# Kernel optimization log

Measured on AMD Instinct MI355X. Metric: run time of the kernel, lower is better.

Reference implementation:

```python
import jax, jax.numpy as jnp
import numpy as np
import math

D = 64  # attention_head_size (hidden_size=64, num_heads=1)
B, N, M = 4, 256, 256
LN_EPS = 1e-5


def setup_inputs() -> dict:
    key = jax.random.key(0)
    ks = jax.random.split(key, 12)
    s = 1.0 / math.sqrt(D)
    return {
        "hidden_states": jax.random.normal(ks[0], (B, N, D), jnp.float32),
        "structure_matrix": jax.random.normal(ks[1], (B, N, M, D), jnp.float32),
        "Wq": jax.random.normal(ks[2], (D, D), jnp.float32) * s,
        "bq": jnp.zeros((D,), jnp.float32),
        "Wk": jax.random.normal(ks[3], (D, D), jnp.float32) * s,
        "bk": jnp.zeros((D,), jnp.float32),
        "Wv": jax.random.normal(ks[4], (D, D), jnp.float32) * s,
        "bv": jnp.zeros((D,), jnp.float32),
        "Wo": jax.random.normal(ks[5], (D, D), jnp.float32) * s,
        "bo": jnp.zeros((D,), jnp.float32),
        "ln_g": jnp.ones((D,), jnp.float32),
        "ln_b": jnp.zeros((D,), jnp.float32),
    }


def reference(hidden_states, structure_matrix, Wq, bq, Wk, bk, Wv, bv, Wo, bo, ln_g, ln_b):
    # hidden_states is unused by the original forward.
    x = structure_matrix  # [B, N, M, D]
    q = x @ Wq.T + bq
    k = x @ Wk.T + bk
    v = x @ Wv.T + bv
    # scores[b,i,a,c] = sum_d k[b,i,a,d] * q[b,i,c,d]  (query broadcast on axis 2)
    scores = jnp.einsum('biad,bicd->biac', k, q) / math.sqrt(D)
    probs = jax.nn.relu(scores)
    # NOTE: original sums (probs + 1e-12) so denom = sum(probs) + M*1e-12
    probs = probs / jnp.sum(probs + 1e-12, axis=-1, keepdims=True)
    # ctx[b,i,a,d] = sum_c probs[b,i,a,c] * v[b,i,c,d]
    ctx = jnp.einsum('biac,bicd->biad', probs, v)
    out = ctx @ Wo.T + bo
    y = out + x
    mu = jnp.mean(y, axis=-1, keepdims=True)
    var = jnp.mean(jnp.square(y - mu), axis=-1, keepdims=True)
    return (y - mu) / jnp.sqrt(var + LN_EPS) * ln_g + ln_b
```

## Files before the change

### kernel.cpp

```cpp
#include <hip/hip_runtime.h>


using bh8   = __attribute__((ext_vector_type(8))) short;
using f32x4 = __attribute__((ext_vector_type(4))) float;

#define MFMA(a, b, c) __builtin_amdgcn_mfma_f32_16x16x32_bf16((a), (b), (c), 0, 0, 0)

#define SQ_STRIDE  72
#define SVT_STRIDE 264
#define SY_STRIDE  72
#define STG_ELTS   (16 * 72)
#define LDS_BYTES  ((256 * SQ_STRIDE * 2 + 64 * SVT_STRIDE + 4 * STG_ELTS) * 2)

__device__ __forceinline__ float bf2f(unsigned short u) {
  union { unsigned int i; float f; } x;
  x.i = ((unsigned int)u) << 16;
  return x.f;
}
__device__ __forceinline__ unsigned short f2bf(float f) {
  union { float f; unsigned int i; } x;
  x.f = f;
  unsigned int u = x.i + 0x7FFFu + ((x.i >> 16) & 1u);
  return (unsigned short)(u >> 16);
}
__device__ __forceinline__ int pkbf(float lo, float hi) {
  return (int)(((unsigned int)f2bf(hi) << 16) | (unsigned int)f2bf(lo));
}

template <int FP32>
__device__ __forceinline__ bh8 g_load8(const void* base, size_t idx) {
  if constexpr (FP32) {
    const float* p = (const float*)base + idx;
    float4 a = *(const float4*)p;
    float4 b = *(const float4*)(p + 4);
    bh8 r;
    r[0] = (short)f2bf(a.x); r[1] = (short)f2bf(a.y);
    r[2] = (short)f2bf(a.z); r[3] = (short)f2bf(a.w);
    r[4] = (short)f2bf(b.x); r[5] = (short)f2bf(b.y);
    r[6] = (short)f2bf(b.z); r[7] = (short)f2bf(b.w);
    return r;
  } else {
    return *(const bh8*)((const unsigned short*)base + idx);
  }
}
template <int FP32>
__device__ __forceinline__ float g_loadf(const void* base, size_t idx) {
  if constexpr (FP32) return ((const float*)base)[idx];
  else return bf2f(((const unsigned short*)base)[idx]);
}

template <int FP32>
__global__ __launch_bounds__(256, 1) void pairattn(
    const void* __restrict__ Xv,
    const void* __restrict__ Wqv, const void* __restrict__ bqv,
    const void* __restrict__ Wkv, const void* __restrict__ bkv,
    const void* __restrict__ Wvv, const void* __restrict__ bvv,
    const void* __restrict__ Wov, const void* __restrict__ bov,
    const void* __restrict__ lngv, const void* __restrict__ lnbv,
    void* __restrict__ Outv) {
  const int tid  = threadIdx.x;
  const int lane = tid & 63;

  {
    const unsigned short* xu = (const unsigned short*)Xv + (lane << 4);
    int huge = 0;
#pragma unroll
    for (int j = 0; j < 16; ++j) {
      unsigned e = ((unsigned)xu[j] >> 7) & 0xFFu;
      huge |= (e >= 0x90u) ? 1 : 0;
    }
    const bool isf32 = (__ballot(huge) != 0ULL);
    if (isf32 != (FP32 != 0)) return;
  }

  extern __shared__ unsigned short sm[];
  unsigned short* sQ  = sm;
  unsigned short* sK  = sQ + 256 * SQ_STRIDE;
  unsigned short* sVt = sK + 256 * SQ_STRIDE;
  unsigned short* sSt = sVt + 64 * SVT_STRIDE;

  const int wv  = tid >> 6;
  const int q4  = lane >> 4;
  const int l16 = lane & 15;
  const int m0w = wv << 6;
  unsigned short* stg = sSt + wv * STG_ELTS;

  bh8 wq[4][2], wk[4][2], wvv[4][2], wo[4][2];
  float bqf[4], bkf[4], bvf[4][4], bof[4], gf[4], lbf[4];
#pragma unroll
  for (int nt = 0; nt < 4; ++nt) {
    const int wrow = (16 * nt + l16) * 64 + 8 * q4;
    wq[nt][0]  = g_load8<FP32>(Wqv, wrow);
    wq[nt][1]  = g_load8<FP32>(Wqv, wrow + 32);
    wk[nt][0]  = g_load8<FP32>(Wkv, wrow);
    wk[nt][1]  = g_load8<FP32>(Wkv, wrow + 32);
    wvv[nt][0] = g_load8<FP32>(Wvv, wrow);
    wvv[nt][1] = g_load8<FP32>(Wvv, wrow + 32);
    wo[nt][0]  = g_load8<FP32>(Wov, wrow);
    wo[nt][1]  = g_load8<FP32>(Wov, wrow + 32);
    const int col = 16 * nt + l16;
    bqf[nt] = g_loadf<FP32>(bqv, col);
    bkf[nt] = g_loadf<FP32>(bkv, col);
    bof[nt] = g_loadf<FP32>(bov, col);
    gf[nt]  = g_loadf<FP32>(lngv, col);
    lbf[nt] = g_loadf<FP32>(lnbv, col);
#pragma unroll
    for (int r = 0; r < 4; ++r)
      bvf[nt][r] = g_loadf<FP32>(bvv, 16 * nt + 4 * q4 + r);
  }

  const int srcA = ((lane & 16) << 1) | l16;
  const int srcB = srcA + 16;
  const bool hsel = (lane & 32) != 0;

#pragma unroll 1
  for (int bi = blockIdx.x; bi < 1024; bi += 256) {
    const size_t xoff = (size_t)bi * 16384;

    {
      bh8 xf[4][2];
#pragma unroll
      for (int mt = 0; mt < 4; ++mt) {
        const size_t xr = xoff + (size_t)(m0w + 16 * mt + l16) * 64 + 8 * q4;
        xf[mt][0] = g_load8<FP32>(Xv, xr);
        xf[mt][1] = g_load8<FP32>(Xv, xr + 32);
      }
#pragma unroll
      for (int mt = 0; mt < 4; ++mt) {
#pragma unroll
        for (int nt = 0; nt < 4; ++nt) {
          f32x4 acc = {0.f, 0.f, 0.f, 0.f};
          acc = MFMA(xf[mt][0], wq[nt][0], acc);
          acc = MFMA(xf[mt][1], wq[nt][1], acc);
#pragma unroll
          for (int r = 0; r < 4; ++r)
            sQ[(m0w + 16 * mt + 4 * q4 + r) * SQ_STRIDE + 16 * nt + l16] =
                f2bf(acc[r] + bqf[nt]);
        }
#pragma unroll
        for (int nt = 0; nt < 4; ++nt) {
          f32x4 acc = {0.f, 0.f, 0.f, 0.f};
          acc = MFMA(xf[mt][0], wk[nt][0], acc);
          acc = MFMA(xf[mt][1], wk[nt][1], acc);
#pragma unroll
          for (int r = 0; r < 4; ++r)
            sK[(m0w + 16 * mt + 4 * q4 + r) * SQ_STRIDE + 16 * nt + l16] =
                f2bf(acc[r] + bkf[nt]);
        }
#pragma unroll
        for (int dt = 0; dt < 4; ++dt) {
          f32x4 acc = {0.f, 0.f, 0.f, 0.f};
          acc = MFMA(wvv[dt][0], xf[mt][0], acc);
          acc = MFMA(wvv[dt][1], xf[mt][1], acc);
#pragma unroll
          for (int r = 0; r < 4; ++r)
            sVt[(16 * dt + 4 * q4 + r) * SVT_STRIDE + m0w + 16 * mt + l16] =
                f2bf(acc[r] + bvf[dt][r]);
        }
      }
    }
    __syncthreads();

    bh8 vfr[8][4];
#pragma unroll
    for (int ct = 0; ct < 8; ++ct)
#pragma unroll
      for (int dt = 0; dt < 4; ++dt)
        vfr[ct][dt] =
            *(const bh8*)(sVt + (16 * dt + l16) * SVT_STRIDE + 32 * ct + 8 * q4);

#pragma unroll 1
    for (int mt = 0; mt < 4; ++mt) {
      const int a0 = m0w + 16 * mt;
      const unsigned short* krow = sK + (a0 + l16) * SQ_STRIDE + 8 * q4;
      bh8 kf0 = *(const bh8*)(krow);
      bh8 kf1 = *(const bh8*)(krow + 32);

      float xres[4][4];
#pragma unroll
      for (int nt = 0; nt < 4; ++nt)
#pragma unroll
        for (int r = 0; r < 4; ++r)
          xres[nt][r] = g_loadf<FP32>(
              Xv, xoff + (size_t)(a0 + 4 * q4 + r) * 64 + 16 * nt + l16);

      f32x4 ctxa[4];
#pragma unroll
      for (int dt = 0; dt < 4; ++dt) ctxa[dt] = (f32x4){0.f, 0.f, 0.f, 0.f};
      float rs = 0.f;

#pragma unroll
      for (int ct = 0; ct < 8; ++ct) {
        int ph0[2], ph1[2];
#pragma unroll
        for (int h = 0; h < 2; ++h) {
          const int c0 = 32 * ct + 16 * h;
          const unsigned short* qrow = sQ + (c0 + l16) * SQ_STRIDE + 8 * q4;
          bh8 qf0 = *(const bh8*)(qrow);
          bh8 qf1 = *(const bh8*)(qrow + 32);
          f32x4 s = {0.f, 0.f, 0.f, 0.f};
          s = MFMA(qf0, kf0, s);
          s = MFMA(qf1, kf1, s);
          float v0 = fmaxf(s[0] * 0.125f, 0.f);
          float v1 = fmaxf(s[1] * 0.125f, 0.f);
          float v2 = fmaxf(s[2] * 0.125f, 0.f);
          float v3 = fmaxf(s[3] * 0.125f, 0.f);
          rs += (v0 + v1) + (v2 + v3);
          if (h == 0) { ph0[0] = pkbf(v0, v1); ph0[1] = pkbf(v2, v3); }
          else        { ph1[0] = pkbf(v0, v1); ph1[1] = pkbf(v2, v3); }
        }
        union { int d[4]; bh8 v; } pfu;
#pragma unroll
        for (int j = 0; j < 4; ++j) {
          const int srcl = (j < 2) ? srcA : srcB;
          int t0, t1;
          if ((j & 1) == 0) { t0 = __shfl(ph0[0], srcl); t1 = __shfl(ph1[0], srcl); }
          else              { t0 = __shfl(ph0[1], srcl); t1 = __shfl(ph1[1], srcl); }
          pfu.d[j] = hsel ? t1 : t0;
        }
#pragma unroll
        for (int dt = 0; dt < 4; ++dt)
          ctxa[dt] = MFMA(vfr[ct][dt], pfu.v, ctxa[dt]);
      }

      rs += __shfl_xor(rs, 16);
      rs += __shfl_xor(rs, 32);
      const float inv = 1.f / (rs + 2.56e-10f);

      int pc[4][2];
#pragma unroll
      for (int dt = 0; dt < 4; ++dt) {
        pc[dt][0] = pkbf(ctxa[dt][0] * inv, ctxa[dt][1] * inv);
        pc[dt][1] = pkbf(ctxa[dt][2] * inv, ctxa[dt][3] * inv);
      }
      union { int d[4]; bh8 v; } cf0u, cf1u;
#pragma unroll
      for (int j = 0; j < 4; ++j) {
        const int srcl = (j < 2) ? srcA : srcB;
        const int jp = j & 1;
        int t0 = __shfl(pc[0][jp], srcl);
        int t1 = __shfl(pc[1][jp], srcl);
        int t2 = __shfl(pc[2][jp], srcl);
        int t3 = __shfl(pc[3][jp], srcl);
        cf0u.d[j] = hsel ? t1 : t0;
        cf1u.d[j] = hsel ? t3 : t2;
      }

      float yv[4][4];
      float s1[4] = {0.f, 0.f, 0.f, 0.f};
      float s2[4] = {0.f, 0.f, 0.f, 0.f};
#pragma unroll
      for (int nt = 0; nt < 4; ++nt) {
        f32x4 o = {0.f, 0.f, 0.f, 0.f};
        o = MFMA(cf0u.v, wo[nt][0], o);
        o = MFMA(cf1u.v, wo[nt][1], o);
#pragma unroll
        for (int r = 0; r < 4; ++r) {
          float y = o[r] + bof[nt] + xres[nt][r];
          yv[nt][r] = y;
          s1[r] += y;
          s2[r] += y * y;
        }
      }
#pragma unroll
      for (int r = 0; r < 4; ++r) {
        s1[r] += __shfl_xor(s1[r], 1);
        s1[r] += __shfl_xor(s1[r], 2);
        s1[r] += __shfl_xor(s1[r], 4);
        s1[r] += __shfl_xor(s1[r], 8);
        s2[r] += __shfl_xor(s2[r], 1);
        s2[r] += __shfl_xor(s2[r], 2);
        s2[r] += __shfl_xor(s2[r], 4);
        s2[r] += __shfl_xor(s2[r], 8);
        const float mu   = s1[r] * 0.015625f;
        const float var  = s2[r] * 0.015625f - mu * mu;
        const float rstd = rsqrtf(var + 1e-5f);
        if constexpr (FP32) {
          float* Outf = (float*)Outv;
#pragma unroll
          for (int nt = 0; nt < 4; ++nt)
            Outf[xoff + (size_t)(a0 + 4 * q4 + r) * 64 + 16 * nt + l16] =
                (yv[nt][r] - mu) * rstd * gf[nt] + lbf[nt];
        } else {
#pragma unroll
          for (int nt = 0; nt < 4; ++nt)
            stg[(4 * q4 + r) * SY_STRIDE + 16 * nt + l16] =
                f2bf((yv[nt][r] - mu) * rstd * gf[nt] + lbf[nt]);
        }
      }
      if constexpr (!FP32) {
        __syncthreads();
        const int row = lane >> 2, seg = lane & 3;
        const unsigned short* yr = stg + row * SY_STRIDE + seg * 8;
        uint4 u0 = *(const uint4*)(yr);
        uint4 u1 = *(const uint4*)(yr + 32);
        unsigned short* orow =
            (unsigned short*)Outv + xoff + (size_t)(a0 + row) * 64 + seg * 8;
        *(uint4*)(orow)      = u0;
        *(uint4*)(orow + 32) = u1;
      }
    }
    __syncthreads();
  }
}

extern "C" void kernel_launch(void* const* d_in, const int* in_sizes, int n_in,
                              void* d_out, int out_size, void* d_ws, size_t ws_size,
                              hipStream_t stream) {
  (void)n_in; (void)d_ws; (void)ws_size; (void)out_size;
  const void* X  = d_in[1];
  const void* Wq = d_in[2];  const void* bq = d_in[3];
  const void* Wk = d_in[4];  const void* bk = d_in[5];
  const void* Wv = d_in[6];  const void* bv = d_in[7];
  const void* Wo = d_in[8];  const void* bo = d_in[9];
  const void* lg = d_in[10]; const void* lb = d_in[11];

  const long long NELT = 16777216LL;
  const long long sz1  = (long long)in_sizes[1];
  bool want_bf16 = true, want_f32 = true;
  if (sz1 == NELT * 2) want_f32 = false;
  else if (sz1 == NELT * 4) want_bf16 = false;

  auto k0 = pairattn<0>;
  auto k1 = pairattn<1>;
  if (want_bf16) {
    hipFuncSetAttribute((const void*)k0, hipFuncAttributeMaxDynamicSharedMemorySize, LDS_BYTES);
    k0<<<256, 256, LDS_BYTES, stream>>>(X, Wq, bq, Wk, bk, Wv, bv, Wo, bo, lg, lb, d_out);
  }
  if (want_f32) {
    hipFuncSetAttribute((const void*)k1, hipFuncAttributeMaxDynamicSharedMemorySize, LDS_BYTES);
    k1<<<256, 256, LDS_BYTES, stream>>>(X, Wq, bq, Wk, bk, Wv, bv, Wo, bo, lg, lb, d_out);
  }
}
```

Measured before the change: 219.6 us.

## Interchange attention loops to keep K fragments resident and stream Q/V per chunk

Swaps the loop nest so the outer loop runs over key/value column chunks (ct) and the inner loop over the four row tiles (mt). All four K fragments and sixteen context accumulators stay in registers, while Q and V fragments are loaded from LDS once per chunk and reused across the four row tiles. Previously Q was reloaded from LDS for every row tile and all 32 V fragments were held in registers. The residual load and normalization move to a separate epilogue loop. The intent is to cut LDS traffic and raise MFMA density, at the cost of more accumulator registers and less overlap of the global residual loads with compute.

```diff
diff --git a/kernel.cpp b/kernel.cpp
--- a/kernel.cpp
+++ b/kernel.cpp
@@ -161,51 +161,51 @@
     }
     __syncthreads();
 
-    bh8 vfr[8][4];
-#pragma unroll
-    for (int ct = 0; ct < 8; ++ct)
+    bh8 kf[4][2];
+#pragma unroll
+    for (int mt = 0; mt < 4; ++mt) {
+      const unsigned short* krow =
+          sK + (m0w + 16 * mt + l16) * SQ_STRIDE + 8 * q4;
+      kf[mt][0] = *(const bh8*)(krow);
+      kf[mt][1] = *(const bh8*)(krow + 32);
+    }
+
+    f32x4 ctxa[4][4];
+    float rs[4] = {0.f, 0.f, 0.f, 0.f};
+#pragma unroll
+    for (int mt = 0; mt < 4; ++mt)
+#pragma unroll
+      for (int dt = 0; dt < 4; ++dt) ctxa[mt][dt] = (f32x4){0.f, 0.f, 0.f, 0.f};
+
+#pragma unroll 1
+    for (int ct = 0; ct < 8; ++ct) {
+      bh8 qf[2][2];
+#pragma unroll
+      for (int h = 0; h < 2; ++h) {
+        const unsigned short* qrow =
+            sQ + (32 * ct + 16 * h + l16) * SQ_STRIDE + 8 * q4;
+        qf[h][0] = *(const bh8*)(qrow);
+        qf[h][1] = *(const bh8*)(qrow + 32);
+      }
+      bh8 vf[4];
 #pragma unroll
       for (int dt = 0; dt < 4; ++dt)
-        vfr[ct][dt] =
+        vf[dt] =
             *(const bh8*)(sVt + (16 * dt + l16) * SVT_STRIDE + 32 * ct + 8 * q4);
 
-#pragma unroll 1
-    for (int mt = 0; mt < 4; ++mt) {
-      const int a0 = m0w + 16 * mt;
-      const unsigned short* krow = sK + (a0 + l16) * SQ_STRIDE + 8 * q4;
-      bh8 kf0 = *(const bh8*)(krow);
-      bh8 kf1 = *(const bh8*)(krow + 32);
-
-      float xres[4][4];
-#pragma unroll
-      for (int nt = 0; nt < 4; ++nt)
-#pragma unroll
-        for (int r = 0; r < 4; ++r)
-          xres[nt][r] = g_loadf<FP32>(
-              Xv, xoff + (size_t)(a0 + 4 * q4 + r) * 64 + 16 * nt + l16);
-
-      f32x4 ctxa[4];
-#pragma unroll
-      for (int dt = 0; dt < 4; ++dt) ctxa[dt] = (f32x4){0.f, 0.f, 0.f, 0.f};
-      float rs = 0.f;
-
-#pragma unroll
-      for (int ct = 0; ct < 8; ++ct) {
+#pragma unroll
+      for (int mt = 0; mt < 4; ++mt) {
         int ph0[2], ph1[2];
 #pragma unroll
         for (int h = 0; h < 2; ++h) {
-          const int c0 = 32 * ct + 16 * h;
-          const unsigned short* qrow = sQ + (c0 + l16) * SQ_STRIDE + 8 * q4;
-          bh8 qf0 = *(const bh8*)(qrow);
-          bh8 qf1 = *(const bh8*)(qrow + 32);
           f32x4 s = {0.f, 0.f, 0.f, 0.f};
-          s = MFMA(qf0, kf0, s);
-          s = MFMA(qf1, kf1, s);
+          s = MFMA(qf[h][0], kf[mt][0], s);
+          s = MFMA(qf[h][1], kf[mt][1], s);
           float v0 = fmaxf(s[0] * 0.125f, 0.f);
           float v1 = fmaxf(s[1] * 0.125f, 0.f);
           float v2 = fmaxf(s[2] * 0.125f, 0.f);
           float v3 = fmaxf(s[3] * 0.125f, 0.f);
-          rs += (v0 + v1) + (v2 + v3);
+          rs[mt] += (v0 + v1) + (v2 + v3);
           if (h == 0) { ph0[0] = pkbf(v0, v1); ph0[1] = pkbf(v2, v3); }
           else        { ph1[0] = pkbf(v0, v1); ph1[1] = pkbf(v2, v3); }
         }
@@ -220,18 +220,32 @@
         }
 #pragma unroll
         for (int dt = 0; dt < 4; ++dt)
-          ctxa[dt] = MFMA(vfr[ct][dt], pfu.v, ctxa[dt]);
-      }
-
-      rs += __shfl_xor(rs, 16);
-      rs += __shfl_xor(rs, 32);
-      const float inv = 1.f / (rs + 2.56e-10f);
+          ctxa[mt][dt] = MFMA(vf[dt], pfu.v, ctxa[mt][dt]);
+      }
+    }
+
+#pragma unroll
+    for (int mt = 0; mt < 4; ++mt) {
+      const int a0 = m0w + 16 * mt;
+
+      float xres[4][4];
+#pragma unroll
+      for (int nt = 0; nt < 4; ++nt)
+#pragma unroll
+        for (int r = 0; r < 4; ++r)
+          xres[nt][r] = g_loadf<FP32>(
+              Xv, xoff + (size_t)(a0 + 4 * q4 + r) * 64 + 16 * nt + l16);
+
+      float rsm = rs[mt];
+      rsm += __shfl_xor(rsm, 16);
+      rsm += __shfl_xor(rsm, 32);
+      const float inv = 1.f / (rsm + 2.56e-10f);
 
       int pc[4][2];
 #pragma unroll
       for (int dt = 0; dt < 4; ++dt) {
-        pc[dt][0] = pkbf(ctxa[dt][0] * inv, ctxa[dt][1] * inv);
-        pc[dt][1] = pkbf(ctxa[dt][2] * inv, ctxa[dt][3] * inv);
+        pc[dt][0] = pkbf(ctxa[mt][dt][0] * inv, ctxa[mt][dt][1] * inv);
+        pc[dt][1] = pkbf(ctxa[mt][dt][2] * inv, ctxa[mt][dt][3] * inv);
       }
       union { int d[4]; bh8 v; } cf0u, cf1u;
 #pragma unroll
```

Result: faster. 208.9 us (-4.9%).
